# Kernel optimization log

Hardware: AMD Instinct MI355X
Metric: run time of the kernel (lower is better)

Reference implementation:

```python
import jax, jax.numpy as jnp
import numpy as np

SCALING = 2.0  # lora alpha / rank
B, S, H = 4, 2048, 4096
N = 4096  # q/k/v out features
R = 16    # lora rank


def setup_inputs() -> dict:
    key = jax.random.key(0)
    ks = jax.random.split(key, 10)
    std_w = 1.0 / np.sqrt(H)
    inp = {
        'X': jax.random.normal(ks[0], (B, S, H), dtype=jnp.float32),
        'QW': jax.random.normal(ks[1], (N, H), dtype=jnp.float32) * std_w,
        'QA': jax.random.normal(ks[2], (R, H), dtype=jnp.float32) * std_w,
        'QB': jax.random.normal(ks[3], (N, R), dtype=jnp.float32) * 0.01,
        'KW': jax.random.normal(ks[4], (N, H), dtype=jnp.float32) * std_w,
        'KA': jax.random.normal(ks[5], (R, H), dtype=jnp.float32) * std_w,
        'KB': jax.random.normal(ks[6], (N, R), dtype=jnp.float32) * 0.01,
        'VW': jax.random.normal(ks[7], (N, H), dtype=jnp.float32) * std_w,
        'VA': jax.random.normal(ks[8], (R, H), dtype=jnp.float32) * std_w,
        'VB': jax.random.normal(ks[9], (N, R), dtype=jnp.float32) * 0.01,
    }
    return inp


def _matmul_lora(X, W, A, Bm, scaling):
    # Y = X @ W.T + scaling * (X @ A.T) @ B.T ; X: [bs, h], W: [n, h], A: [r, h], B: [n, r]
    base = jnp.einsum('bsh,nh->bsn', X, W)
    lora = jnp.einsum('bsr,nr->bsn', jnp.einsum('bsh,rh->bsr', X, A), Bm)
    return base + scaling * lora


def reference(X, QW, QA, QB, KW, KA, KB, VW, VA, VB):
    Q = _matmul_lora(X, QW, QA, QB, SCALING)
    K = _matmul_lora(X, KW, KA, KB, SCALING)
    V = _matmul_lora(X, VW, VA, VB, SCALING)
    return (Q, K, V)
```

## Files before the change

### kernel.cpp

```cpp
#include <hip/hip_runtime.h>


typedef unsigned short u16;
typedef __attribute__((ext_vector_type(4))) float  f32x4;
typedef __attribute__((ext_vector_type(8))) __bf16 bf16x8;
typedef __attribute__((ext_vector_type(8))) short  s16x8;

#define MDIM 8192
#define NDIM 4096
#define KDIM 4096

__device__ __forceinline__ u16 f2bf(float f) {
    union { float f; unsigned int u; } v;
    v.f = f;
    unsigned int r = v.u + 0x7FFFu + ((v.u >> 16) & 1u);
    return (u16)(r >> 16);
}

__global__ void __launch_bounds__(256) cvt_x_kernel(const float* __restrict__ X,
                                                    u16* __restrict__ Xb, int nvec8) {
    int stride = gridDim.x * blockDim.x;
    for (int i = blockIdx.x * blockDim.x + threadIdx.x; i < nvec8; i += stride) {
        f32x4 x0 = ((const f32x4*)X)[2 * i];
        f32x4 x1 = ((const f32x4*)X)[2 * i + 1];
        s16x8 o;
        o[0] = (short)f2bf(x0[0]); o[1] = (short)f2bf(x0[1]);
        o[2] = (short)f2bf(x0[2]); o[3] = (short)f2bf(x0[3]);
        o[4] = (short)f2bf(x1[0]); o[5] = (short)f2bf(x1[1]);
        o[6] = (short)f2bf(x1[2]); o[7] = (short)f2bf(x1[3]);
        ((s16x8*)Xb)[i] = o;
    }
}

__global__ void __launch_bounds__(256) merge_w_kernel(const float* __restrict__ W,
                                                      const float* __restrict__ A,
                                                      const float* __restrict__ Bm,
                                                      u16* __restrict__ Wb) {
    __shared__ float As[16][64];
    const int t  = threadIdx.x;
    const int hb = blockIdx.x * 64;
    const int nb = blockIdx.y * 128;

    {
        int r = t >> 4, c = (t & 15) * 4;
        *(f32x4*)&As[r][c] = *(const f32x4*)&A[r * 4096 + hb + c];
    }
    __syncthreads();

    const int hl = (t & 7) * 8;
    const int n0 = nb + (t >> 3) * 4;

    float bv[4][16];
    float s[4][8];
#pragma unroll
    for (int i = 0; i < 4; i++) {
        const float* br = &Bm[(size_t)(n0 + i) * 16];
#pragma unroll
        for (int r = 0; r < 16; r++) bv[i][r] = 2.0f * br[r];
        f32x4 w0 = *(const f32x4*)&W[(size_t)(n0 + i) * 4096 + hb + hl];
        f32x4 w1 = *(const f32x4*)&W[(size_t)(n0 + i) * 4096 + hb + hl + 4];
        s[i][0] = w0[0]; s[i][1] = w0[1]; s[i][2] = w0[2]; s[i][3] = w0[3];
        s[i][4] = w1[0]; s[i][5] = w1[1]; s[i][6] = w1[2]; s[i][7] = w1[3];
    }
#pragma unroll
    for (int r = 0; r < 16; r++) {
        f32x4 a0 = *(const f32x4*)&As[r][hl];
        f32x4 a1 = *(const f32x4*)&As[r][hl + 4];
#pragma unroll
        for (int i = 0; i < 4; i++) {
            s[i][0] += bv[i][r] * a0[0]; s[i][1] += bv[i][r] * a0[1];
            s[i][2] += bv[i][r] * a0[2]; s[i][3] += bv[i][r] * a0[3];
            s[i][4] += bv[i][r] * a1[0]; s[i][5] += bv[i][r] * a1[1];
            s[i][6] += bv[i][r] * a1[2]; s[i][7] += bv[i][r] * a1[3];
        }
    }
#pragma unroll
    for (int i = 0; i < 4; i++) {
        s16x8 o;
#pragma unroll
        for (int j = 0; j < 8; j++) o[j] = (short)f2bf(s[i][j]);
        *(s16x8*)&Wb[(size_t)(n0 + i) * 4096 + hb + hl] = o;
    }
}


#define BM 256
#define BN 256
#define BK 64
#define NKT (KDIM / BK)

#define BAR() __builtin_amdgcn_s_barrier()
#define WAIT_LGKM0() asm volatile("s_waitcnt lgkmcnt(0)" ::: "memory")
#define WAIT_VM(n) asm volatile("s_waitcnt vmcnt(" #n ")" ::: "memory")
#define PRIO(p) __builtin_amdgcn_s_setprio(p)

__global__ void __launch_bounds__(512, 2) gemm8_kernel(const u16* __restrict__ Xb,
                                                       const u16* __restrict__ Wb,
                                                       float* __restrict__ out) {
    extern __shared__ char lds[];

    const int t    = threadIdx.x;
    const int lane = t & 63;
    const int w    = t >> 6;
    const int wr   = w >> 2;
    const int wn   = w & 3;
    const int lr   = lane & 15;
    const int lkq  = lane >> 4;
    const int lr7  = lr & 7;

    int wg = blockIdx.x;
    wg = (wg & 7) * 192 + (wg >> 3);
    const int z  = wg >> 9;
    const int r_ = wg & 511;
    const int nT = r_ & 15;
    const int mT = r_ >> 4;
    const int mBase = mT * BM;
    const int nBase = nT * BN;

    const u16* Wp = Wb + (size_t)z * NDIM * KDIM;
    const char* gA = (const char*)Xb + (size_t)mBase * (KDIM * 2);
    const char* gB = (const char*)Wp + (size_t)nBase * (KDIM * 2);

    char* ldsA0 = lds;
    char* ldsA1 = lds + 32768;
    char* ldsB0 = lds + 65536;
    char* ldsB1 = lds + 98304;

    const int blkrow = lane >> 3;
    const int colswz = ((lane & 7) ^ blkrow) << 4;
    const size_t stg0 = (size_t)(((w << 1) | 0) * 8 + blkrow) * (KDIM * 2) + colswz;
    const size_t stg1 = (size_t)(((w << 1) | 1) * 8 + blkrow) * (KDIM * 2) + colswz;
    const int ldsStg0 = (((w << 1) | 0) << 10) + lane * 16;
    const int ldsStg1 = (((w << 1) | 1) << 10) + lane * 16;

#define STAGE(ldsTile, gtile, h, kt)                                              \
  { __builtin_amdgcn_global_load_lds(                                             \
        (const __attribute__((address_space(1))) void*)((gtile) + stg0 +          \
            (size_t)(h) * (128 * KDIM * 2) + (size_t)(kt) * 128),                 \
        (__attribute__((address_space(3))) void*)((ldsTile) + (h) * 16384 + ldsStg0), \
        16, 0, 0);                                                                \
    __builtin_amdgcn_global_load_lds(                                             \
        (const __attribute__((address_space(1))) void*)((gtile) + stg1 +          \
            (size_t)(h) * (128 * KDIM * 2) + (size_t)(kt) * 128),                 \
        (__attribute__((address_space(3))) void*)((ldsTile) + (h) * 16384 + ldsStg1), \
        16, 0, 0); }

    const int csA = (lkq << 4) ^ (lr7 << 4);
    const int rA0 = (wr * 128 + lr) * 128;
    const int rB0 = (wn * 64 + lr) * 128;
#define RD_A(tile, mi, kk) (*(const bf16x8*)((tile) + rA0 + (mi) * 2048 + (((kk) << 6) ^ csA)))
#define RD_B(tile, ni, kk) (*(const bf16x8*)((tile) + rB0 + (ni) * 2048 + (((kk) << 6) ^ csA)))

    f32x4 acc[8][4] = {};
    bf16x8 aR1[4][2], aR2[4][2], bR[4][2];

#define MFMA_Q(AF, mbase, nbase)                                                   \
    PRIO(1);                                                                       \
    _Pragma("unroll") for (int mi = 0; mi < 4; ++mi)                               \
    _Pragma("unroll") for (int ni = 0; ni < 2; ++ni)                               \
    _Pragma("unroll") for (int kk = 0; kk < 2; ++kk)                               \
      acc[(mbase) + mi][(nbase) + ni] = __builtin_amdgcn_mfma_f32_16x16x32_bf16(   \
          AF[mi][kk], bR[(nbase) + ni][kk], acc[(mbase) + mi][(nbase) + ni], 0, 0, 0); \
    PRIO(0);

#define PH1(pA, pB, STG)                                                           \
  { _Pragma("unroll") for (int mi = 0; mi < 4; ++mi) {                             \
      aR1[mi][0] = RD_A(pA, mi, 0); aR1[mi][1] = RD_A(pA, mi, 1); }                \
    _Pragma("unroll") for (int ni = 0; ni < 4; ++ni) {                             \
      bR[ni][0] = RD_B(pB, ni, 0); bR[ni][1] = RD_B(pB, ni, 1); }                  \
    STG; BAR(); WAIT_LGKM0(); MFMA_Q(aR1, 0, 0) BAR(); }

#define PH2(pA, STG)                                                               \
  { aR2[0][0] = RD_A(pA, 4, 0); aR2[0][1] = RD_A(pA, 4, 1);                        \
    aR2[1][0] = RD_A(pA, 5, 0); aR2[1][1] = RD_A(pA, 5, 1);                        \
    STG; BAR(); WAIT_LGKM0(); MFMA_Q(aR1, 0, 2) BAR(); }

#define PH3(pA, STG)                                                               \
  { aR2[2][0] = RD_A(pA, 6, 0); aR2[2][1] = RD_A(pA, 6, 1);                        \
    aR2[3][0] = RD_A(pA, 7, 0); aR2[3][1] = RD_A(pA, 7, 1);                        \
    STG; BAR(); WAIT_LGKM0(); MFMA_Q(aR2, 4, 0) BAR(); }

#define PH4(STG, VMW)                                                              \
  { STG; VMW; BAR(); WAIT_LGKM0(); MFMA_Q(aR2, 4, 2) BAR(); }

    STAGE(ldsA0, gA, 0, 0); STAGE(ldsA0, gA, 1, 0);
    STAGE(ldsB0, gB, 0, 0); STAGE(ldsB0, gB, 1, 0);
    STAGE(ldsB1, gB, 0, 1); STAGE(ldsB1, gB, 1, 1);
    STAGE(ldsA1, gA, 0, 1);
    WAIT_VM(6);
    BAR();

    for (int i = 0; i < 31; ++i) {
        const int tt = 2 * i;
        PH1(ldsA0, ldsB0, STAGE(ldsA1, gA, 1, tt + 1));
        PH2(ldsA0,        STAGE(ldsB0, gB, 0, tt + 2));
        PH3(ldsA0,        STAGE(ldsB0, gB, 1, tt + 2));
        PH4(              STAGE(ldsA0, gA, 0, tt + 2), WAIT_VM(6));
        PH1(ldsA1, ldsB1, STAGE(ldsA0, gA, 1, tt + 2));
        PH2(ldsA1,        STAGE(ldsB1, gB, 0, tt + 3));
        PH3(ldsA1,        STAGE(ldsB1, gB, 1, tt + 3));
        PH4(              STAGE(ldsA1, gA, 0, tt + 3), WAIT_VM(6));
    }

    PH1(ldsA0, ldsB0, STAGE(ldsA1, gA, 1, 63));
    PH2(ldsA0, );
    PH3(ldsA0, );
    PH4(, WAIT_VM(0));
    PH1(ldsA1, ldsB1, );
    PH2(ldsA1, );
    PH3(ldsA1, );
    PH4(, );

    float* C = out + (size_t)z * MDIM * NDIM;
#pragma unroll
    for (int mi = 0; mi < 8; ++mi) {
#pragma unroll
        for (int ni = 0; ni < 4; ++ni) {
            const int col  = nBase + wn * 64 + ni * 16 + lr;
            const int row0 = mBase + wr * 128 + mi * 16 + lkq * 4;
            f32x4 v = acc[mi][ni];
#pragma unroll
            for (int j = 0; j < 4; ++j)
                C[(size_t)(row0 + j) * NDIM + col] = v[j];
        }
    }
}

extern "C" void kernel_launch(void* const* d_in, const int* in_sizes, int n_in,
                              void* d_out, int out_size, void* d_ws, size_t ws_size,
                              hipStream_t stream) {
    const float* X  = (const float*)d_in[0];
    const float* QW = (const float*)d_in[1];
    const float* QA = (const float*)d_in[2];
    const float* QB = (const float*)d_in[3];
    const float* KW = (const float*)d_in[4];
    const float* KA = (const float*)d_in[5];
    const float* KB = (const float*)d_in[6];
    const float* VW = (const float*)d_in[7];
    const float* VA = (const float*)d_in[8];
    const float* VB = (const float*)d_in[9];
    float* out = (float*)d_out;

    u16* Xb = (u16*)d_ws;
    u16* Wb = (u16*)((char*)d_ws + (size_t)MDIM * KDIM * 2);

    static bool attr_done = false;
    if (!attr_done) {
        (void)hipFuncSetAttribute((const void*)gemm8_kernel,
                                  hipFuncAttributeMaxDynamicSharedMemorySize, 131072);
        attr_done = true;
    }

    cvt_x_kernel<<<2048, 256, 0, stream>>>(X, Xb, (MDIM * KDIM) / 8);

    dim3 wgrid(4096 / 64, 4096 / 128);
    merge_w_kernel<<<wgrid, 256, 0, stream>>>(QW, QA, QB, Wb + (size_t)0 * NDIM * KDIM);
    merge_w_kernel<<<wgrid, 256, 0, stream>>>(KW, KA, KB, Wb + (size_t)1 * NDIM * KDIM);
    merge_w_kernel<<<wgrid, 256, 0, stream>>>(VW, VA, VB, Wb + (size_t)2 * NDIM * KDIM);

    gemm8_kernel<<<dim3(16 * 32 * 3), dim3(512), 131072, stream>>>(Xb, Wb, out);
}
```

Measured before the change: 802.1 us.

## Switch GEMM to 32x32x16 MFMA with reworked LDS schedule and fused weight merge

Replaces the 16x16x32 bf16 MFMA tiling with 32x32x16 instructions (f32x16 accumulators), which changes the LDS read pattern, the register fragment layout and the four-phase pipeline. Next-tile A/B fragments are now prefetched in phase 4 and the explicit lgkmcnt waits are removed. The three per-projection weight-merge launches become one launch with a z grid dimension, and the attribute set runs on every call. Larger MFMAs need fewer LDS reads per FLOP but raise register pressure, and relying on compiler-inserted waits could change the overlap.

```diff
diff --git a/kernel.cpp b/kernel.cpp
--- a/kernel.cpp
+++ b/kernel.cpp
@@ -2,9 +2,10 @@
 
 
 typedef unsigned short u16;
-typedef __attribute__((ext_vector_type(4))) float  f32x4;
-typedef __attribute__((ext_vector_type(8))) __bf16 bf16x8;
-typedef __attribute__((ext_vector_type(8))) short  s16x8;
+typedef __attribute__((ext_vector_type(4)))  float  f32x4;
+typedef __attribute__((ext_vector_type(16))) float  f32x16;
+typedef __attribute__((ext_vector_type(8)))  __bf16 bf16x8;
+typedef __attribute__((ext_vector_type(8)))  short  s16x8;
 
 #define MDIM 8192
 #define NDIM 4096
@@ -32,10 +33,22 @@
     }
 }
 
-__global__ void __launch_bounds__(256) merge_w_kernel(const float* __restrict__ W,
-                                                      const float* __restrict__ A,
-                                                      const float* __restrict__ Bm,
-                                                      u16* __restrict__ Wb) {
+__global__ void __launch_bounds__(256) merge_w3_kernel(const float* __restrict__ QW,
+                                                       const float* __restrict__ QA,
+                                                       const float* __restrict__ QB,
+                                                       const float* __restrict__ KW,
+                                                       const float* __restrict__ KA,
+                                                       const float* __restrict__ KB,
+                                                       const float* __restrict__ VW,
+                                                       const float* __restrict__ VA,
+                                                       const float* __restrict__ VB,
+                                                       u16* __restrict__ WbAll) {
+    const int z = blockIdx.z;
+    const float* W  = (z == 0) ? QW : (z == 1) ? KW : VW;
+    const float* A  = (z == 0) ? QA : (z == 1) ? KA : VA;
+    const float* Bm = (z == 0) ? QB : (z == 1) ? KB : VB;
+    u16* Wb = WbAll + (size_t)z * NDIM * KDIM;
+
     __shared__ float As[16][64];
     const int t  = threadIdx.x;
     const int hb = blockIdx.x * 64;
@@ -87,10 +100,8 @@
 #define BM 256
 #define BN 256
 #define BK 64
-#define NKT (KDIM / BK)
 
 #define BAR() __builtin_amdgcn_s_barrier()
-#define WAIT_LGKM0() asm volatile("s_waitcnt lgkmcnt(0)" ::: "memory")
 #define WAIT_VM(n) asm volatile("s_waitcnt vmcnt(" #n ")" ::: "memory")
 #define PRIO(p) __builtin_amdgcn_s_setprio(p)
 
@@ -104,9 +115,9 @@
     const int w    = t >> 6;
     const int wr   = w >> 2;
     const int wn   = w & 3;
-    const int lr   = lane & 15;
-    const int lkq  = lane >> 4;
-    const int lr7  = lr & 7;
+    const int l31  = lane & 31;
+    const int hi   = lane >> 5;
+    const int swz  = l31 & 7;
 
     int wg = blockIdx.x;
     wg = (wg & 7) * 192 + (wg >> 3);
@@ -145,83 +156,92 @@
         (__attribute__((address_space(3))) void*)((ldsTile) + (h) * 16384 + ldsStg1), \
         16, 0, 0); }
 
-    const int csA = (lkq << 4) ^ (lr7 << 4);
-    const int rA0 = (wr * 128 + lr) * 128;
-    const int rB0 = (wn * 64 + lr) * 128;
-#define RD_A(tile, mi, kk) (*(const bf16x8*)((tile) + rA0 + (mi) * 2048 + (((kk) << 6) ^ csA)))
-#define RD_B(tile, ni, kk) (*(const bf16x8*)((tile) + rB0 + (ni) * 2048 + (((kk) << 6) ^ csA)))
-
-    f32x4 acc[8][4] = {};
-    bf16x8 aR1[4][2], aR2[4][2], bR[4][2];
-
-#define MFMA_Q(AF, mbase, nbase)                                                   \
+    const int rA0 = (wr * 128 + l31) * 128;
+    const int rB0 = (wn * 64 + l31) * 128;
+#define RD_A(tile, mi, ks) (*(const bf16x8*)((tile) + rA0 + (mi) * 4096 + (((((ks) << 1) | hi) ^ swz) << 4)))
+#define RD_B(tile, ni, ks) (*(const bf16x8*)((tile) + rB0 + (ni) * 4096 + (((((ks) << 1) | hi) ^ swz) << 4)))
+
+    f32x16 acc[4][2] = {};
+    bf16x8 aLo[2][4], aHi[2][4], bb[2][4];
+
+#define MFMA_Q(AF, mbase, nidx)                                                    \
     PRIO(1);                                                                       \
-    _Pragma("unroll") for (int mi = 0; mi < 4; ++mi)                               \
-    _Pragma("unroll") for (int ni = 0; ni < 2; ++ni)                               \
-    _Pragma("unroll") for (int kk = 0; kk < 2; ++kk)                               \
-      acc[(mbase) + mi][(nbase) + ni] = __builtin_amdgcn_mfma_f32_16x16x32_bf16(   \
-          AF[mi][kk], bR[(nbase) + ni][kk], acc[(mbase) + mi][(nbase) + ni], 0, 0, 0); \
+    _Pragma("unroll") for (int ks = 0; ks < 4; ++ks)                               \
+    _Pragma("unroll") for (int mi = 0; mi < 2; ++mi)                               \
+      acc[(mbase) + mi][nidx] = __builtin_amdgcn_mfma_f32_32x32x16_bf16(           \
+          AF[mi][ks], bb[nidx][ks], acc[(mbase) + mi][nidx], 0, 0, 0);             \
     PRIO(0);
 
-#define PH1(pA, pB, STG)                                                           \
-  { _Pragma("unroll") for (int mi = 0; mi < 4; ++mi) {                             \
-      aR1[mi][0] = RD_A(pA, mi, 0); aR1[mi][1] = RD_A(pA, mi, 1); }                \
-    _Pragma("unroll") for (int ni = 0; ni < 4; ++ni) {                             \
-      bR[ni][0] = RD_B(pB, ni, 0); bR[ni][1] = RD_B(pB, ni, 1); }                  \
-    STG; BAR(); WAIT_LGKM0(); MFMA_Q(aR1, 0, 0) BAR(); }
+#define PH1(pB, STG)                                                               \
+  { _Pragma("unroll") for (int ks = 0; ks < 4; ++ks) bb[1][ks] = RD_B(pB, 1, ks);  \
+    STG; BAR(); MFMA_Q(aLo, 0, 0) BAR(); }
 
 #define PH2(pA, STG)                                                               \
-  { aR2[0][0] = RD_A(pA, 4, 0); aR2[0][1] = RD_A(pA, 4, 1);                        \
-    aR2[1][0] = RD_A(pA, 5, 0); aR2[1][1] = RD_A(pA, 5, 1);                        \
-    STG; BAR(); WAIT_LGKM0(); MFMA_Q(aR1, 0, 2) BAR(); }
-
-#define PH3(pA, STG)                                                               \
-  { aR2[2][0] = RD_A(pA, 6, 0); aR2[2][1] = RD_A(pA, 6, 1);                        \
-    aR2[3][0] = RD_A(pA, 7, 0); aR2[3][1] = RD_A(pA, 7, 1);                        \
-    STG; BAR(); WAIT_LGKM0(); MFMA_Q(aR2, 4, 0) BAR(); }
-
-#define PH4(STG, VMW)                                                              \
-  { STG; VMW; BAR(); WAIT_LGKM0(); MFMA_Q(aR2, 4, 2) BAR(); }
+  { _Pragma("unroll") for (int mi = 0; mi < 2; ++mi)                               \
+    _Pragma("unroll") for (int ks = 0; ks < 4; ++ks)                               \
+      aHi[mi][ks] = RD_A(pA, 2 + mi, ks);                                          \
+    STG; BAR(); MFMA_Q(aLo, 0, 1) BAR(); }
+
+#define PH3(STG)                                                                   \
+  { STG; BAR(); MFMA_Q(aHi, 2, 0) BAR(); }
+
+#define PH4(pAn, pBn, STG, VMW)                                                    \
+  { STG; VMW; BAR();                                                               \
+    _Pragma("unroll") for (int mi = 0; mi < 2; ++mi)                               \
+    _Pragma("unroll") for (int ks = 0; ks < 4; ++ks)                               \
+      aLo[mi][ks] = RD_A(pAn, mi, ks);                                             \
+    _Pragma("unroll") for (int ks = 0; ks < 4; ++ks) bb[0][ks] = RD_B(pBn, 0, ks); \
+    MFMA_Q(aHi, 2, 1) BAR(); }
+
+#define PH4F()                                                                     \
+  { BAR(); MFMA_Q(aHi, 2, 1) }
 
     STAGE(ldsA0, gA, 0, 0); STAGE(ldsA0, gA, 1, 0);
     STAGE(ldsB0, gB, 0, 0); STAGE(ldsB0, gB, 1, 0);
     STAGE(ldsB1, gB, 0, 1); STAGE(ldsB1, gB, 1, 1);
-    STAGE(ldsA1, gA, 0, 1);
-    WAIT_VM(6);
+    WAIT_VM(4);
     BAR();
+#pragma unroll
+    for (int mi = 0; mi < 2; ++mi)
+#pragma unroll
+        for (int ks = 0; ks < 4; ++ks) aLo[mi][ks] = RD_A(ldsA0, mi, ks);
+#pragma unroll
+    for (int ks = 0; ks < 4; ++ks) bb[0][ks] = RD_B(ldsB0, 0, ks);
 
     for (int i = 0; i < 31; ++i) {
         const int tt = 2 * i;
-        PH1(ldsA0, ldsB0, STAGE(ldsA1, gA, 1, tt + 1));
-        PH2(ldsA0,        STAGE(ldsB0, gB, 0, tt + 2));
-        PH3(ldsA0,        STAGE(ldsB0, gB, 1, tt + 2));
-        PH4(              STAGE(ldsA0, gA, 0, tt + 2), WAIT_VM(6));
-        PH1(ldsA1, ldsB1, STAGE(ldsA0, gA, 1, tt + 2));
-        PH2(ldsA1,        STAGE(ldsB1, gB, 0, tt + 3));
-        PH3(ldsA1,        STAGE(ldsB1, gB, 1, tt + 3));
-        PH4(              STAGE(ldsA1, gA, 0, tt + 3), WAIT_VM(6));
-    }
-
-    PH1(ldsA0, ldsB0, STAGE(ldsA1, gA, 1, 63));
-    PH2(ldsA0, );
-    PH3(ldsA0, );
-    PH4(, WAIT_VM(0));
-    PH1(ldsA1, ldsB1, );
+        PH1(ldsB0,        STAGE(ldsA1, gA, 0, tt + 1));
+        PH2(ldsA0,        STAGE(ldsA1, gA, 1, tt + 1));
+        PH3(              STAGE(ldsB0, gB, 0, tt + 2));
+        PH4(ldsA1, ldsB1, STAGE(ldsB0, gB, 1, tt + 2), WAIT_VM(4));
+        PH1(ldsB1,        STAGE(ldsA0, gA, 0, tt + 2));
+        PH2(ldsA1,        STAGE(ldsA0, gA, 1, tt + 2));
+        PH3(              STAGE(ldsB1, gB, 0, tt + 3));
+        PH4(ldsA0, ldsB0, STAGE(ldsB1, gB, 1, tt + 3), WAIT_VM(4));
+    }
+
+    PH1(ldsB0,        STAGE(ldsA1, gA, 0, 63));
+    PH2(ldsA0,        STAGE(ldsA1, gA, 1, 63));
+    PH3( );
+    PH4(ldsA1, ldsB1, , WAIT_VM(0));
+    PH1(ldsB1, );
     PH2(ldsA1, );
-    PH3(ldsA1, );
-    PH4(, );
+    PH3( );
+    PH4F();
 
     float* C = out + (size_t)z * MDIM * NDIM;
 #pragma unroll
-    for (int mi = 0; mi < 8; ++mi) {
-#pragma unroll
-        for (int ni = 0; ni < 4; ++ni) {
-            const int col  = nBase + wn * 64 + ni * 16 + lr;
-            const int row0 = mBase + wr * 128 + mi * 16 + lkq * 4;
-            f32x4 v = acc[mi][ni];
-#pragma unroll
-            for (int j = 0; j < 4; ++j)
-                C[(size_t)(row0 + j) * NDIM + col] = v[j];
+    for (int mi = 0; mi < 4; ++mi) {
+#pragma unroll
+        for (int ni = 0; ni < 2; ++ni) {
+            const int col  = nBase + wn * 64 + ni * 32 + l31;
+            const int rowb = mBase + wr * 128 + mi * 32 + 4 * hi;
+            f32x16 v = acc[mi][ni];
+#pragma unroll
+            for (int reg = 0; reg < 16; ++reg) {
+                const int row = rowb + (reg & 3) + 8 * (reg >> 2);
+                C[(size_t)row * NDIM + col] = v[reg];
+            }
         }
     }
 }
@@ -244,19 +264,13 @@
     u16* Xb = (u16*)d_ws;
     u16* Wb = (u16*)((char*)d_ws + (size_t)MDIM * KDIM * 2);
 
-    static bool attr_done = false;
-    if (!attr_done) {
-        (void)hipFuncSetAttribute((const void*)gemm8_kernel,
-                                  hipFuncAttributeMaxDynamicSharedMemorySize, 131072);
-        attr_done = true;
-    }
+    (void)hipFuncSetAttribute((const void*)gemm8_kernel,
+                              hipFuncAttributeMaxDynamicSharedMemorySize, 131072);
 
     cvt_x_kernel<<<2048, 256, 0, stream>>>(X, Xb, (MDIM * KDIM) / 8);
 
-    dim3 wgrid(4096 / 64, 4096 / 128);
-    merge_w_kernel<<<wgrid, 256, 0, stream>>>(QW, QA, QB, Wb + (size_t)0 * NDIM * KDIM);
-    merge_w_kernel<<<wgrid, 256, 0, stream>>>(KW, KA, KB, Wb + (size_t)1 * NDIM * KDIM);
-    merge_w_kernel<<<wgrid, 256, 0, stream>>>(VW, VA, VB, Wb + (size_t)2 * NDIM * KDIM);
+    dim3 wgrid(4096 / 64, 4096 / 128, 3);
+    merge_w3_kernel<<<wgrid, 256, 0, stream>>>(QW, QA, QB, KW, KA, KB, VW, VA, VB, Wb);
 
     gemm8_kernel<<<dim3(16 * 32 * 3), dim3(512), 131072, stream>>>(Xb, Wb, out);
 }
```

Measured after the change: 1.126 ms. 40.4% more time.

## Software-pipeline LDS fragment loads across k-tiles and fuse LoRA weight-merge launches

Applied to the files above, without the earlier changes.

The GEMM main loop is rescheduled so the next k-tile's A and B register fragments are read from LDS during the last MFMA phase of the current tile, instead of at the start of each tile. The explicit lgkmcnt(0) waits are dropped, leaving the compiler to insert LDS waits, and the global-to-LDS staging order and vmcnt thresholds are reordered to match. Separately, the three per-projection weight-merge kernels become one launch with a z grid dimension. The aim is to hide LDS latency behind MFMA work and cut launch overhead, at the cost of a more delicate buffer-hazard schedule and possibly higher register pressure.

```diff
diff --git a/kernel.cpp b/kernel.cpp
--- a/kernel.cpp
+++ b/kernel.cpp
@@ -32,10 +32,22 @@
     }
 }
 
-__global__ void __launch_bounds__(256) merge_w_kernel(const float* __restrict__ W,
-                                                      const float* __restrict__ A,
-                                                      const float* __restrict__ Bm,
-                                                      u16* __restrict__ Wb) {
+__global__ void __launch_bounds__(256) merge_w3_kernel(const float* __restrict__ QW,
+                                                       const float* __restrict__ QA,
+                                                       const float* __restrict__ QB,
+                                                       const float* __restrict__ KW,
+                                                       const float* __restrict__ KA,
+                                                       const float* __restrict__ KB,
+                                                       const float* __restrict__ VW,
+                                                       const float* __restrict__ VA,
+                                                       const float* __restrict__ VB,
+                                                       u16* __restrict__ WbAll) {
+    const int z = blockIdx.z;
+    const float* W  = (z == 0) ? QW : (z == 1) ? KW : VW;
+    const float* A  = (z == 0) ? QA : (z == 1) ? KA : VA;
+    const float* Bm = (z == 0) ? QB : (z == 1) ? KB : VB;
+    u16* Wb = WbAll + (size_t)z * NDIM * KDIM;
+
     __shared__ float As[16][64];
     const int t  = threadIdx.x;
     const int hb = blockIdx.x * 64;
@@ -87,10 +99,8 @@
 #define BM 256
 #define BN 256
 #define BK 64
-#define NKT (KDIM / BK)
 
 #define BAR() __builtin_amdgcn_s_barrier()
-#define WAIT_LGKM0() asm volatile("s_waitcnt lgkmcnt(0)" ::: "memory")
 #define WAIT_VM(n) asm volatile("s_waitcnt vmcnt(" #n ")" ::: "memory")
 #define PRIO(p) __builtin_amdgcn_s_setprio(p)
 
@@ -163,53 +173,73 @@
           AF[mi][kk], bR[(nbase) + ni][kk], acc[(mbase) + mi][(nbase) + ni], 0, 0, 0); \
     PRIO(0);
 
-#define PH1(pA, pB, STG)                                                           \
-  { _Pragma("unroll") for (int mi = 0; mi < 4; ++mi) {                             \
-      aR1[mi][0] = RD_A(pA, mi, 0); aR1[mi][1] = RD_A(pA, mi, 1); }                \
-    _Pragma("unroll") for (int ni = 0; ni < 4; ++ni) {                             \
-      bR[ni][0] = RD_B(pB, ni, 0); bR[ni][1] = RD_B(pB, ni, 1); }                  \
-    STG; BAR(); WAIT_LGKM0(); MFMA_Q(aR1, 0, 0) BAR(); }
-
-#define PH2(pA, STG)                                                               \
+#define PH1(pA, STG)                                                               \
   { aR2[0][0] = RD_A(pA, 4, 0); aR2[0][1] = RD_A(pA, 4, 1);                        \
     aR2[1][0] = RD_A(pA, 5, 0); aR2[1][1] = RD_A(pA, 5, 1);                        \
-    STG; BAR(); WAIT_LGKM0(); MFMA_Q(aR1, 0, 2) BAR(); }
-
-#define PH3(pA, STG)                                                               \
+    STG; BAR(); MFMA_Q(aR1, 0, 0) BAR(); }
+
+#define PH2(pA, STG)                                                               \
   { aR2[2][0] = RD_A(pA, 6, 0); aR2[2][1] = RD_A(pA, 6, 1);                        \
     aR2[3][0] = RD_A(pA, 7, 0); aR2[3][1] = RD_A(pA, 7, 1);                        \
-    STG; BAR(); WAIT_LGKM0(); MFMA_Q(aR2, 4, 0) BAR(); }
-
-#define PH4(STG, VMW)                                                              \
-  { STG; VMW; BAR(); WAIT_LGKM0(); MFMA_Q(aR2, 4, 2) BAR(); }
+    STG; BAR(); MFMA_Q(aR2, 4, 0) BAR(); }
+
+#undef PH2
+#define PH2(pA, STG)                                                               \
+  { aR2[2][0] = RD_A(pA, 6, 0); aR2[2][1] = RD_A(pA, 6, 1);                        \
+    aR2[3][0] = RD_A(pA, 7, 0); aR2[3][1] = RD_A(pA, 7, 1);                        \
+    STG; BAR(); MFMA_Q(aR1, 0, 2) BAR(); }
+
+#define PH3(STG)                                                                   \
+  { STG; BAR(); MFMA_Q(aR2, 4, 0) BAR(); }
+
+#define PH4(pAn, pBn, STG, VMW)                                                    \
+  { STG; VMW; BAR();                                                               \
+    _Pragma("unroll") for (int mi = 0; mi < 4; ++mi) {                             \
+      aR1[mi][0] = RD_A(pAn, mi, 0); aR1[mi][1] = RD_A(pAn, mi, 1); }              \
+    bR[0][0] = RD_B(pBn, 0, 0); bR[0][1] = RD_B(pBn, 0, 1);                        \
+    bR[1][0] = RD_B(pBn, 1, 0); bR[1][1] = RD_B(pBn, 1, 1);                        \
+    MFMA_Q(aR2, 4, 2)                                                              \
+    bR[2][0] = RD_B(pBn, 2, 0); bR[2][1] = RD_B(pBn, 2, 1);                        \
+    bR[3][0] = RD_B(pBn, 3, 0); bR[3][1] = RD_B(pBn, 3, 1);                        \
+    BAR(); }
+
+#define PH4F()                                                                     \
+  { BAR(); MFMA_Q(aR2, 4, 2) }
 
     STAGE(ldsA0, gA, 0, 0); STAGE(ldsA0, gA, 1, 0);
     STAGE(ldsB0, gB, 0, 0); STAGE(ldsB0, gB, 1, 0);
     STAGE(ldsB1, gB, 0, 1); STAGE(ldsB1, gB, 1, 1);
-    STAGE(ldsA1, gA, 0, 1);
-    WAIT_VM(6);
+    WAIT_VM(4);
     BAR();
+#pragma unroll
+    for (int mi = 0; mi < 4; ++mi) {
+        aR1[mi][0] = RD_A(ldsA0, mi, 0); aR1[mi][1] = RD_A(ldsA0, mi, 1);
+    }
+#pragma unroll
+    for (int ni = 0; ni < 4; ++ni) {
+        bR[ni][0] = RD_B(ldsB0, ni, 0); bR[ni][1] = RD_B(ldsB0, ni, 1);
+    }
 
     for (int i = 0; i < 31; ++i) {
-        const int tt = 2 * i;
-        PH1(ldsA0, ldsB0, STAGE(ldsA1, gA, 1, tt + 1));
-        PH2(ldsA0,        STAGE(ldsB0, gB, 0, tt + 2));
-        PH3(ldsA0,        STAGE(ldsB0, gB, 1, tt + 2));
-        PH4(              STAGE(ldsA0, gA, 0, tt + 2), WAIT_VM(6));
-        PH1(ldsA1, ldsB1, STAGE(ldsA0, gA, 1, tt + 2));
-        PH2(ldsA1,        STAGE(ldsB1, gB, 0, tt + 3));
-        PH3(ldsA1,        STAGE(ldsB1, gB, 1, tt + 3));
-        PH4(              STAGE(ldsA1, gA, 0, tt + 3), WAIT_VM(6));
-    }
-
-    PH1(ldsA0, ldsB0, STAGE(ldsA1, gA, 1, 63));
-    PH2(ldsA0, );
-    PH3(ldsA0, );
-    PH4(, WAIT_VM(0));
-    PH1(ldsA1, ldsB1, );
+        const int T = 2 * i;
+        PH1(ldsA0,        STAGE(ldsA1, gA, 0, T + 1));
+        PH2(ldsA0,        STAGE(ldsA1, gA, 1, T + 1));
+        PH3(              STAGE(ldsB0, gB, 0, T + 2));
+        PH4(ldsA1, ldsB1, STAGE(ldsB0, gB, 1, T + 2), WAIT_VM(4));
+        PH1(ldsA1,        STAGE(ldsA0, gA, 0, T + 2));
+        PH2(ldsA1,        STAGE(ldsA0, gA, 1, T + 2));
+        PH3(              STAGE(ldsB1, gB, 0, T + 3));
+        PH4(ldsA0, ldsB0, STAGE(ldsB1, gB, 1, T + 3), WAIT_VM(4));
+    }
+
+    PH1(ldsA0,        STAGE(ldsA1, gA, 0, 63));
+    PH2(ldsA0,        STAGE(ldsA1, gA, 1, 63));
+    PH3( );
+    PH4(ldsA1, ldsB1, , WAIT_VM(0));
+    PH1(ldsA1, );
     PH2(ldsA1, );
-    PH3(ldsA1, );
-    PH4(, );
+    PH3( );
+    PH4F();
 
     float* C = out + (size_t)z * MDIM * NDIM;
 #pragma unroll
@@ -244,19 +274,13 @@
     u16* Xb = (u16*)d_ws;
     u16* Wb = (u16*)((char*)d_ws + (size_t)MDIM * KDIM * 2);
 
-    static bool attr_done = false;
-    if (!attr_done) {
-        (void)hipFuncSetAttribute((const void*)gemm8_kernel,
-                                  hipFuncAttributeMaxDynamicSharedMemorySize, 131072);
-        attr_done = true;
-    }
+    (void)hipFuncSetAttribute((const void*)gemm8_kernel,
+                              hipFuncAttributeMaxDynamicSharedMemorySize, 131072);
 
     cvt_x_kernel<<<2048, 256, 0, stream>>>(X, Xb, (MDIM * KDIM) / 8);
 
-    dim3 wgrid(4096 / 64, 4096 / 128);
-    merge_w_kernel<<<wgrid, 256, 0, stream>>>(QW, QA, QB, Wb + (size_t)0 * NDIM * KDIM);
-    merge_w_kernel<<<wgrid, 256, 0, stream>>>(KW, KA, KB, Wb + (size_t)1 * NDIM * KDIM);
-    merge_w_kernel<<<wgrid, 256, 0, stream>>>(VW, VA, VB, Wb + (size_t)2 * NDIM * KDIM);
+    dim3 wgrid(4096 / 64, 4096 / 128, 3);
+    merge_w3_kernel<<<wgrid, 256, 0, stream>>>(QW, QA, QB, KW, KA, KB, VW, VA, VB, Wb);
 
     gemm8_kernel<<<dim3(16 * 32 * 3), dim3(512), 131072, stream>>>(Xb, Wb, out);
 }
```

Result: slower. 854.0 us (+6.5%).
